# Performance work log

Measured on AMD Instinct MI355X. Metric: run time of the kernel, lower is better.

## Reference

```python
import jax, jax.numpy as jnp
import numpy as np

HEADS = 16
DIM_HEAD = 64
SCALE = DIM_HEAD ** -0.5


def setup_inputs() -> dict:
    key = jax.random.key(0)
    k1, k2, k3, k4 = jax.random.split(key, 4)
    b, n, dim = 2, 2048, 1024
    inner = HEADS * DIM_HEAD  # 1024
    x = jax.random.normal(k1, (b, n, dim), dtype=jnp.float32)
    mask = jax.random.randint(k2, (b, n), 0, 2, dtype=jnp.int32)
    Wqkv = jax.random.normal(k3, (dim, inner), dtype=jnp.float32) * (dim ** -0.5)
    Wout = jax.random.normal(k4, (inner, dim), dtype=jnp.float32) * (inner ** -0.5)
    bout = jnp.zeros((dim,), dtype=jnp.float32)
    return {"x": x, "mask": mask, "Wqkv": Wqkv, "Wout": Wout, "bout": bout}


def reference(x, mask, Wqkv, Wout, bout):
    b, n, _ = x.shape
    # shared projection: w acts as q = k = v (CRATE subspace attention)
    w = jnp.einsum('bnd,de->bne', x, Wqkv)
    w = w.reshape(b, n, HEADS, DIM_HEAD).transpose(0, 2, 1, 3)  # b h n d
    dots = jnp.einsum('bhid,bhjd->bhij', w, w) * SCALE           # b h n n
    attn = jax.nn.softmax(dots, axis=-1)
    # post-softmax multiplicative masking (mask=1 zeros the column)
    m = mask[:, None, None, :].astype(attn.dtype)
    attn = attn * (1.0 - m)
    out = jnp.einsum('bhij,bhjd->bhid', attn, w)                 # b h n d
    out = out.transpose(0, 2, 1, 3).reshape(b, n, HEADS * DIM_HEAD)
    return jnp.einsum('bne,ed->bnd', out, Wout) + bout
```

## Files before the change

kernel.cpp:

```cpp
#include <hip/hip_runtime.h>
#include <hip/hip_bf16.h>
#include <stdint.h>

typedef unsigned short u16;
typedef unsigned int u32;
typedef __bf16 bf16x8 __attribute__((ext_vector_type(8)));
typedef float f32x4 __attribute__((ext_vector_type(4)));

#define AS1 __attribute__((address_space(1)))
#define AS3 __attribute__((address_space(3)))

__device__ __forceinline__ void async16(const u16* g, u16* l) {
  __builtin_amdgcn_global_load_lds((const AS1 uint32_t*)(const void*)g,
                                   (AS3 uint32_t*)l, 16, 0, 0);
}

__device__ __forceinline__ u16 f2bf(float v) {
  union { __hip_bfloat16 b; u16 u; } c; c.b = __float2bfloat16(v); return c.u;
}

__device__ __forceinline__ uint4 pack8(float4 lo, float4 hi) {
  uint4 q;
  q.x = (u32)f2bf(lo.x) | ((u32)f2bf(lo.y) << 16);
  q.y = (u32)f2bf(lo.z) | ((u32)f2bf(lo.w) << 16);
  q.z = (u32)f2bf(hi.x) | ((u32)f2bf(hi.y) << 16);
  q.w = (u32)f2bf(hi.z) | ((u32)f2bf(hi.w) << 16);
  return q;
}

__global__ void cvt_x(const float* __restrict__ in, u16* __restrict__ out) {
  int i = (blockIdx.x * 256 + threadIdx.x) * 8;
  float4 lo = *(const float4*)(in + i);
  float4 hi = *(const float4*)(in + i + 4);
  *(uint4*)(out + i) = pack8(lo, hi);
}

__global__ void transpose1024_cvt2(const float* __restrict__ in0, u16* __restrict__ out0,
                                   const float* __restrict__ in1, u16* __restrict__ out1) {
  const float* in = blockIdx.z ? in1 : in0;
  u16* out = blockIdx.z ? out1 : out0;
  __shared__ u16 tile[32][33];
  int tx = threadIdx.x, ty = threadIdx.y;
  int c0 = blockIdx.x * 32, r0 = blockIdx.y * 32;
#pragma unroll
  for (int i = 0; i < 32; i += 8)
    tile[ty + i][tx] = f2bf(in[(size_t)(r0 + ty + i) * 1024 + c0 + tx]);
  __syncthreads();
#pragma unroll
  for (int i = 0; i < 32; i += 8)
    out[(size_t)(c0 + ty + i) * 1024 + r0 + tx] = tile[tx][ty + i];
}

__global__ void scale_transpose_v(const u16* __restrict__ w, const int* __restrict__ mask,
                                  u16* __restrict__ Vt) {
  __shared__ u16 tile[32][33];
  const int tx = threadIdx.x, ty = threadIdx.y;
  const int j0 = blockIdx.x * 32, d0 = blockIdx.y * 32;
  const int bh = blockIdx.z, b = bh >> 4, hc = (bh & 15) * 64;
#pragma unroll
  for (int i = 0; i < 32; i += 8) {
    int j = j0 + ty + i;
    u16 v = w[(size_t)(b * 2048 + j) * 1024 + hc + d0 + tx];
    tile[ty + i][tx] = mask[b * 2048 + j] ? (u16)0 : v;
  }
  __syncthreads();
#pragma unroll
  for (int i = 0; i < 32; i += 8)
    Vt[((size_t)bh * 64 + d0 + ty + i) * 2048 + j0 + tx] = tile[tx][ty + i];
}

template<bool OUT_F32>
__launch_bounds__(256)
__global__ void gemm_bt(const u16* __restrict__ A, const u16* __restrict__ BT,
                        void* __restrict__ Cp, const float* __restrict__ bias,
                        int M, int N, int K) {
  __shared__ __align__(16) u16 As[2][128 * 32];
  __shared__ __align__(16) u16 Bs[2][64 * 32];
  const int t = threadIdx.x;
  const int lane = t & 63, wave = t >> 6;
  const int m0 = blockIdx.x * 128, n0 = blockIdx.y * 64;
  const int wm = (wave & 1) * 64, wn = (wave >> 1) * 32;
  const int lrow = lane & 15, quad = lane >> 4;

  f32x4 acc[4][2] = {};

  const int ar = t >> 2, ac = (t & 3) * 8;
  const u16* gA = A + (size_t)(m0 + ar) * K + ac;
  const u16* gB = BT + (size_t)(n0 + ar) * K + ac;

  for (int k0 = 0; k0 < K; k0 += 64) {
    async16(gA + k0,                       &As[0][t * 8]);
    async16(gA + k0 + (size_t)64 * K,      &As[0][t * 8 + 2048]);
    async16(gA + k0 + 32,                  &As[1][t * 8]);
    async16(gA + k0 + 32 + (size_t)64 * K, &As[1][t * 8 + 2048]);
    async16(gB + k0,                       &Bs[0][t * 8]);
    async16(gB + k0 + 32,                  &Bs[1][t * 8]);
    __syncthreads();

#pragma unroll
    for (int kk = 0; kk < 2; kk++) {
      bf16x8 af[4], bfr[2];
#pragma unroll
      for (int i = 0; i < 4; i++)
        af[i] = *(const bf16x8*)&As[kk][(wm + i * 16 + lrow) * 32 + quad * 8];
#pragma unroll
      for (int j = 0; j < 2; j++)
        bfr[j] = *(const bf16x8*)&Bs[kk][(wn + j * 16 + lrow) * 32 + quad * 8];
#pragma unroll
      for (int i = 0; i < 4; i++)
#pragma unroll
        for (int j = 0; j < 2; j++)
          acc[i][j] = __builtin_amdgcn_mfma_f32_16x16x32_bf16(af[i], bfr[j], acc[i][j], 0, 0, 0);
    }
    __syncthreads();
  }

  float bv[2];
#pragma unroll
  for (int j = 0; j < 2; j++)
    bv[j] = bias ? bias[n0 + wn + j * 16 + lrow] : 0.f;

#pragma unroll
  for (int i = 0; i < 4; i++) {
#pragma unroll
    for (int r = 0; r < 4; r++) {
      int row = m0 + wm + i * 16 + quad * 4 + r;
#pragma unroll
      for (int j = 0; j < 2; j++) {
        size_t ci = (size_t)row * N + n0 + wn + j * 16 + lrow;
        float v = acc[i][j][r] + bv[j];
        if (OUT_F32) ((float*)Cp)[ci] = v;
        else ((u16*)Cp)[ci] = f2bf(v);
      }
    }
  }
}

#define SV 72
#define C1 0.18033688f
#define C2 -28.853901f
__launch_bounds__(256)
__global__ void attn_kernel(const u16* __restrict__ w, const u16* __restrict__ Vt,
                            u16* __restrict__ y) {
  __shared__ __align__(16) u16 Ws[64 * SV];
  __shared__ __align__(16) u16 VTs[64 * SV];
  __shared__ __align__(16) u16 P[4][16 * SV];
  const int t = threadIdx.x, lane = t & 63, wave = t >> 6;
  const int lrow = lane & 15, quad = lane >> 4;
  const int bh = blockIdx.y, b = bh >> 4, h = bh & 15;
  const int q0 = blockIdx.x * 64;
  const size_t rowb = (size_t)b * 2048;
  const int hc = h * 64;
  u16* Pw = P[wave];

  const int sr = t >> 2, sc = (t & 3) * 16;
  const u16* kg = &w[(rowb + sr) * 1024 + hc + sc];
  const u16* vg = &Vt[((size_t)bh * 64 + sr) * 2048 + sc];

  bf16x8 qf0, qf1;
  {
    const size_t qrow = rowb + q0 + wave * 16 + lrow;
    qf0 = *(const bf16x8*)&w[qrow * 1024 + hc + quad * 8];
    qf1 = *(const bf16x8*)&w[qrow * 1024 + hc + 32 + quad * 8];
  }

  uint4 ka = *(const uint4*)kg, kb = *(const uint4*)(kg + 8);
  uint4 va = *(const uint4*)vg, vc = *(const uint4*)(vg + 8);

  f32x4 o[4] = {};
  float lrun[4] = {0.f, 0.f, 0.f, 0.f};

  for (int j0 = 0; j0 < 2048; j0 += 64) {
    __syncthreads();
    *(uint4*)&Ws[sr * SV + sc]      = ka;
    *(uint4*)&Ws[sr * SV + sc + 8]  = kb;
    *(uint4*)&VTs[sr * SV + sc]     = va;
    *(uint4*)&VTs[sr * SV + sc + 8] = vc;
    __syncthreads();

    if (j0 + 64 < 2048) {
      const u16* kn = kg + (size_t)(j0 + 64) * 1024;
      const u16* vn = vg + j0 + 64;
      ka = *(const uint4*)kn; kb = *(const uint4*)(kn + 8);
      va = *(const uint4*)vn; vc = *(const uint4*)(vn + 8);
    }

    f32x4 st[4];
#pragma unroll
    for (int jt = 0; jt < 4; jt++) {
      bf16x8 kf0 = *(const bf16x8*)&Ws[(jt * 16 + lrow) * SV + quad * 8];
      bf16x8 kf1 = *(const bf16x8*)&Ws[(jt * 16 + lrow) * SV + 32 + quad * 8];
      f32x4 z = {};
      z = __builtin_amdgcn_mfma_f32_16x16x32_bf16(qf0, kf0, z, 0, 0, 0);
      z = __builtin_amdgcn_mfma_f32_16x16x32_bf16(qf1, kf1, z, 0, 0, 0);
      st[jt] = z;
    }

#pragma unroll
    for (int jt = 0; jt < 4; jt++) {
#pragma unroll
      for (int r = 0; r < 4; r++) {
        float e = exp2f(fmaf(st[jt][r], C1, C2));
        lrun[r] += e;
        Pw[(quad * 4 + r) * SV + jt * 16 + lrow] = f2bf(e);
      }
    }

    bf16x8 pa0 = *(const bf16x8*)&Pw[lrow * SV + quad * 8];
    bf16x8 pa1 = *(const bf16x8*)&Pw[lrow * SV + 32 + quad * 8];
#pragma unroll
    for (int dt = 0; dt < 4; dt++) {
      bf16x8 vb0 = *(const bf16x8*)&VTs[(dt * 16 + lrow) * SV + quad * 8];
      bf16x8 vb1 = *(const bf16x8*)&VTs[(dt * 16 + lrow) * SV + 32 + quad * 8];
      o[dt] = __builtin_amdgcn_mfma_f32_16x16x32_bf16(pa0, vb0, o[dt], 0, 0, 0);
      o[dt] = __builtin_amdgcn_mfma_f32_16x16x32_bf16(pa1, vb1, o[dt], 0, 0, 0);
    }
  }

#pragma unroll
  for (int r = 0; r < 4; r++) {
    float l = lrun[r];
#pragma unroll
    for (int s = 8; s >= 1; s >>= 1)
      l += __shfl_xor(l, s, 64);
    float inv = 1.f / l;
    const size_t orow = rowb + q0 + wave * 16 + quad * 4 + r;
#pragma unroll
    for (int dt = 0; dt < 4; dt++)
      y[orow * 1024 + hc + dt * 16 + lrow] = f2bf(o[dt][r] * inv);
  }
}

extern "C" void kernel_launch(void* const* d_in, const int* in_sizes, int n_in,
                              void* d_out, int out_size, void* d_ws, size_t ws_size,
                              hipStream_t stream) {
  const float* x    = (const float*)d_in[0];
  const int* mask   = (const int*)d_in[1];
  const float* Wqkv = (const float*)d_in[2];
  const float* Wout = (const float*)d_in[3];
  const float* bout = (const float*)d_in[4];
  float* out = (float*)d_out;

  u16* w     = (u16*)d_ws;
  u16* y     = w + 4096 * 1024;
  u16* WqkvT = y + 4096 * 1024;
  u16* WoutT = WqkvT + 1024 * 1024;
  u16* Vt    = WoutT + 1024 * 1024;
  u16* xb    = y;

  cvt_x<<<2048, 256, 0, stream>>>(x, xb);
  transpose1024_cvt2<<<dim3(32, 32, 2), dim3(32, 8), 0, stream>>>(Wqkv, WqkvT, Wout, WoutT);
  gemm_bt<false><<<dim3(32, 16), 256, 0, stream>>>(xb, WqkvT, w, nullptr, 4096, 1024, 1024);
  scale_transpose_v<<<dim3(64, 2, 32), dim3(32, 8), 0, stream>>>(w, mask, Vt);
  attn_kernel<<<dim3(32, 32), 256, 0, stream>>>(w, Vt, y);
  gemm_bt<true><<<dim3(32, 16), 256, 0, stream>>>(y, WoutT, out, bout, 4096, 1024, 1024);
}
```

Baseline: 191.8 us.

## Rewrite attention with 32x32 MFMA, register-resident P and async double-buffered K/V

The attention kernel moves from 16x16x32 to 32x32x16 MFMAs and computes S transposed, so the exponentiated probabilities can be packed and rearranged in registers with v_permlane32_swap rather than staged through LDS. K and V tiles are loaded with global_load_lds into double-buffered, XOR-swizzled shared memory, which overlaps the next tile's fetch with compute and removes padding. Each block now handles 128 queries (32 per wave), halving the grid, and the normalizer is redistributed with ds_bpermute at the end. It adds permlane and swizzle complexity and leaves fewer blocks in flight.

After: 194.1 us. No clear change (+1.2%).

```diff
diff --git a/kernel.cpp b/kernel.cpp
--- a/kernel.cpp
+++ b/kernel.cpp
@@ -6,6 +6,8 @@
 typedef unsigned int u32;
 typedef __bf16 bf16x8 __attribute__((ext_vector_type(8)));
 typedef float f32x4 __attribute__((ext_vector_type(4)));
+typedef float f32x16 __attribute__((ext_vector_type(16)));
+typedef u32 u32x4 __attribute__((ext_vector_type(4)));
 
 #define AS1 __attribute__((address_space(1)))
 #define AS3 __attribute__((address_space(3)))
@@ -17,6 +19,14 @@
 
 __device__ __forceinline__ u16 f2bf(float v) {
   union { __hip_bfloat16 b; u16 u; } c; c.b = __float2bfloat16(v); return c.u;
+}
+
+__device__ __forceinline__ u32 pkbf(float a, float b) {
+  return (u32)f2bf(a) | ((u32)f2bf(b) << 16);
+}
+
+__device__ __forceinline__ void swap32(u32 &a, u32 &b) {
+  asm("v_permlane32_swap_b32 %0, %1" : "+v"(a), "+v"(b));
 }
 
 __device__ __forceinline__ uint4 pack8(float4 lo, float4 hi) {
@@ -136,98 +146,103 @@
   }
 }
 
-#define SV 72
 #define C1 0.18033688f
 #define C2 -28.853901f
 __launch_bounds__(256)
 __global__ void attn_kernel(const u16* __restrict__ w, const u16* __restrict__ Vt,
                             u16* __restrict__ y) {
-  __shared__ __align__(16) u16 Ws[64 * SV];
-  __shared__ __align__(16) u16 VTs[64 * SV];
-  __shared__ __align__(16) u16 P[4][16 * SV];
-  const int t = threadIdx.x, lane = t & 63, wave = t >> 6;
-  const int lrow = lane & 15, quad = lane >> 4;
-  const int bh = blockIdx.y, b = bh >> 4, h = bh & 15;
-  const int q0 = blockIdx.x * 64;
+  __shared__ __align__(16) u16 Ws[2][64 * 64];
+  __shared__ __align__(16) u16 VTs[2][64 * 64];
+  const int t = threadIdx.x, lane = t & 63, wv = t >> 6;
+  const int ql = lane & 31, hi = lane >> 5, swz = ql & 7;
+  const int bh = blockIdx.y, b = bh >> 4, hc = (bh & 15) * 64;
+  const int q0 = blockIdx.x * 128;
   const size_t rowb = (size_t)b * 2048;
-  const int hc = h * 64;
-  u16* Pw = P[wave];
-
-  const int sr = t >> 2, sc = (t & 3) * 16;
-  const u16* kg = &w[(rowb + sr) * 1024 + hc + sc];
-  const u16* vg = &Vt[((size_t)bh * 64 + sr) * 2048 + sc];
-
-  bf16x8 qf0, qf1;
+
+  const int skey = t >> 3;
+  const int scl = ((t & 7) ^ (skey & 7)) * 8;
+  const u16* kg = w + rowb * 1024 + hc;
+  const u16* vg = Vt + (size_t)bh * 64 * 2048;
+
+  bf16x8 qf[4];
   {
-    const size_t qrow = rowb + q0 + wave * 16 + lrow;
-    qf0 = *(const bf16x8*)&w[qrow * 1024 + hc + quad * 8];
-    qf1 = *(const bf16x8*)&w[qrow * 1024 + hc + 32 + quad * 8];
-  }
-
-  uint4 ka = *(const uint4*)kg, kb = *(const uint4*)(kg + 8);
-  uint4 va = *(const uint4*)vg, vc = *(const uint4*)(vg + 8);
-
-  f32x4 o[4] = {};
-  float lrun[4] = {0.f, 0.f, 0.f, 0.f};
-
+    const size_t qrow = rowb + q0 + wv * 32 + ql;
+#pragma unroll
+    for (int ks = 0; ks < 4; ks++)
+      qf[ks] = *(const bf16x8*)&w[qrow * 1024 + hc + ks * 16 + hi * 8];
+  }
+
+  f32x16 o0 = {}, o1 = {};
+  float lrun = 0.f;
+
+#define STAGE(buf, j0s) do { \
+    async16(kg + (size_t)((j0s) + skey) * 1024 + scl,       &Ws[buf][t * 8]); \
+    async16(kg + (size_t)((j0s) + skey + 32) * 1024 + scl,  &Ws[buf][2048 + t * 8]); \
+    async16(vg + (size_t)skey * 2048 + (j0s) + scl,         &VTs[buf][t * 8]); \
+    async16(vg + (size_t)(skey + 32) * 2048 + (j0s) + scl,  &VTs[buf][2048 + t * 8]); \
+  } while (0)
+
+  STAGE(0, 0);
+  __syncthreads();
+
+  int cur = 0;
   for (int j0 = 0; j0 < 2048; j0 += 64) {
+    if (j0 + 64 < 2048) STAGE(cur ^ 1, j0 + 64);
+
+    u32x4 pa[4];
+#pragma unroll
+    for (int g = 0; g < 2; g++) {
+      f32x16 p = {};
+#pragma unroll
+      for (int ks = 0; ks < 4; ks++) {
+        bf16x8 af = *(const bf16x8*)
+            &Ws[cur][(g * 32 + ql) * 64 + (((ks * 2 + hi) ^ swz) * 8)];
+        p = __builtin_amdgcn_mfma_f32_32x32x16_bf16(af, qf[ks], p, 0, 0, 0);
+      }
+      float e[16];
+#pragma unroll
+      for (int r = 0; r < 16; r++) {
+        e[r] = exp2f(fmaf(p[r], C1, C2));
+        lrun += e[r];
+      }
+      u32 a0 = pkbf(e[0], e[1]),   b0 = pkbf(e[4], e[5]);   swap32(a0, b0);
+      u32 a1 = pkbf(e[2], e[3]),   b1 = pkbf(e[6], e[7]);   swap32(a1, b1);
+      u32 a2 = pkbf(e[8], e[9]),   b2 = pkbf(e[12], e[13]); swap32(a2, b2);
+      u32 a3 = pkbf(e[10], e[11]), b3 = pkbf(e[14], e[15]); swap32(a3, b3);
+      u32x4 f0 = {a0, a1, b0, b1};
+      u32x4 f1 = {a2, a3, b2, b3};
+      pa[2 * g + 0] = f0;
+      pa[2 * g + 1] = f1;
+    }
+
+    __builtin_amdgcn_s_setprio(1);
+#pragma unroll
+    for (int ks = 0; ks < 4; ks++) {
+      union { u32x4 u; bf16x8 bf; } cv; cv.u = pa[ks];
+      bf16x8 vb0 = *(const bf16x8*)
+          &VTs[cur][ql * 64 + (((ks * 2 + hi) ^ swz) * 8)];
+      bf16x8 vb1 = *(const bf16x8*)
+          &VTs[cur][(32 + ql) * 64 + (((ks * 2 + hi) ^ swz) * 8)];
+      o0 = __builtin_amdgcn_mfma_f32_32x32x16_bf16(cv.bf, vb0, o0, 0, 0, 0);
+      o1 = __builtin_amdgcn_mfma_f32_32x32x16_bf16(cv.bf, vb1, o1, 0, 0, 0);
+    }
+    __builtin_amdgcn_s_setprio(0);
+
     __syncthreads();
-    *(uint4*)&Ws[sr * SV + sc]      = ka;
-    *(uint4*)&Ws[sr * SV + sc + 8]  = kb;
-    *(uint4*)&VTs[sr * SV + sc]     = va;
-    *(uint4*)&VTs[sr * SV + sc + 8] = vc;
-    __syncthreads();
-
-    if (j0 + 64 < 2048) {
-      const u16* kn = kg + (size_t)(j0 + 64) * 1024;
-      const u16* vn = vg + j0 + 64;
-      ka = *(const uint4*)kn; kb = *(const uint4*)(kn + 8);
-      va = *(const uint4*)vn; vc = *(const uint4*)(vn + 8);
-    }
-
-    f32x4 st[4];
-#pragma unroll
-    for (int jt = 0; jt < 4; jt++) {
-      bf16x8 kf0 = *(const bf16x8*)&Ws[(jt * 16 + lrow) * SV + quad * 8];
-      bf16x8 kf1 = *(const bf16x8*)&Ws[(jt * 16 + lrow) * SV + 32 + quad * 8];
-      f32x4 z = {};
-      z = __builtin_amdgcn_mfma_f32_16x16x32_bf16(qf0, kf0, z, 0, 0, 0);
-      z = __builtin_amdgcn_mfma_f32_16x16x32_bf16(qf1, kf1, z, 0, 0, 0);
-      st[jt] = z;
-    }
-
-#pragma unroll
-    for (int jt = 0; jt < 4; jt++) {
-#pragma unroll
-      for (int r = 0; r < 4; r++) {
-        float e = exp2f(fmaf(st[jt][r], C1, C2));
-        lrun[r] += e;
-        Pw[(quad * 4 + r) * SV + jt * 16 + lrow] = f2bf(e);
-      }
-    }
-
-    bf16x8 pa0 = *(const bf16x8*)&Pw[lrow * SV + quad * 8];
-    bf16x8 pa1 = *(const bf16x8*)&Pw[lrow * SV + 32 + quad * 8];
-#pragma unroll
-    for (int dt = 0; dt < 4; dt++) {
-      bf16x8 vb0 = *(const bf16x8*)&VTs[(dt * 16 + lrow) * SV + quad * 8];
-      bf16x8 vb1 = *(const bf16x8*)&VTs[(dt * 16 + lrow) * SV + 32 + quad * 8];
-      o[dt] = __builtin_amdgcn_mfma_f32_16x16x32_bf16(pa0, vb0, o[dt], 0, 0, 0);
-      o[dt] = __builtin_amdgcn_mfma_f32_16x16x32_bf16(pa1, vb1, o[dt], 0, 0, 0);
-    }
-  }
-
-#pragma unroll
-  for (int r = 0; r < 4; r++) {
-    float l = lrun[r];
-#pragma unroll
-    for (int s = 8; s >= 1; s >>= 1)
-      l += __shfl_xor(l, s, 64);
-    float inv = 1.f / l;
-    const size_t orow = rowb + q0 + wave * 16 + quad * 4 + r;
-#pragma unroll
-    for (int dt = 0; dt < 4; dt++)
-      y[orow * 1024 + hc + dt * 16 + lrow] = f2bf(o[dt][r] * inv);
+    cur ^= 1;
+  }
+#undef STAGE
+
+  lrun += __shfl_xor(lrun, 32, 64);
+  const float inv = 1.f / lrun;
+#pragma unroll
+  for (int r = 0; r < 16; r++) {
+    const int qo = (r & 3) + 8 * (r >> 2) + 4 * hi;
+    const float iv = __int_as_float(
+        __builtin_amdgcn_ds_bpermute(qo * 4, __float_as_int(inv)));
+    const size_t orow = rowb + q0 + wv * 32 + qo;
+    y[orow * 1024 + hc + ql]      = f2bf(o0[r] * iv);
+    y[orow * 1024 + hc + 32 + ql] = f2bf(o1[r] * iv);
   }
 }
 
@@ -252,6 +267,6 @@
   transpose1024_cvt2<<<dim3(32, 32, 2), dim3(32, 8), 0, stream>>>(Wqkv, WqkvT, Wout, WoutT);
   gemm_bt<false><<<dim3(32, 16), 256, 0, stream>>>(xb, WqkvT, w, nullptr, 4096, 1024, 1024);
   scale_transpose_v<<<dim3(64, 2, 32), dim3(32, 8), 0, stream>>>(w, mask, Vt);
-  attn_kernel<<<dim3(32, 32), 256, 0, stream>>>(w, Vt, y);
+  attn_kernel<<<dim3(16, 32), 256, 0, stream>>>(w, Vt, y);
   gemm_bt<true><<<dim3(32, 16), 256, 0, stream>>>(y, WoutT, out, bout, 4096, 1024, 1024);
 }
```
